# Optimization experiments

Hardware: AMD Instinct MI355X
Metric: run time of the kernel (lower is better)

## Reference

```python
import jax, jax.numpy as jnp
import numpy as np
import math

DIM = 1024
NUM_HEADS = 16
QUANTUM_HEADS = 2
HEAD_DIM = DIM // NUM_HEADS          # 64
TRAD_HEADS = NUM_HEADS - QUANTUM_HEADS  # 14
B, S = 1, 1024
STEPS = 2048
LN_EPS = 1e-5


def setup_inputs() -> dict:
    key = jax.random.key(0)
    ks = jax.random.split(key, 10)
    hd2 = 2 * HEAD_DIM
    return {
        "x": jax.random.normal(ks[0], (B, S, DIM), jnp.float32),
        # to_quantum_state: Linear(head_dim -> 2*head_dim) + LayerNorm + Tanh (shared across quantum heads)
        "qs_W": jax.random.normal(ks[1], (hd2, HEAD_DIM), jnp.float32) / math.sqrt(HEAD_DIM),
        "qs_b": jnp.zeros((hd2,), jnp.float32),
        "ln_g": jnp.ones((hd2,), jnp.float32),
        "ln_b": jnp.zeros((hd2,), jnp.float32),
        # per-quantum-head scalars
        "q_freq": jax.random.normal(ks[2], (QUANTUM_HEADS,), jnp.float32) * 0.02,
        "q_shift": jax.random.normal(ks[3], (QUANTUM_HEADS,), jnp.float32) * 0.02,
        # traditional head projections (no bias)
        "Wq": jax.random.normal(ks[4], (TRAD_HEADS * HEAD_DIM, DIM), jnp.float32) / math.sqrt(DIM),
        "Wk": jax.random.normal(ks[5], (TRAD_HEADS * HEAD_DIM, DIM), jnp.float32) / math.sqrt(DIM),
        "Wv": jax.random.normal(ks[6], (TRAD_HEADS * HEAD_DIM, DIM), jnp.float32) / math.sqrt(DIM),
        # output projection (with bias)
        "Wo": jax.random.normal(ks[7], (DIM, DIM), jnp.float32) / math.sqrt(DIM),
        "bo": jnp.zeros((DIM,), jnp.float32),
    }


def _layernorm(h, g, b):
    mu = jnp.mean(h, axis=-1, keepdims=True)
    var = jnp.mean(jnp.square(h - mu), axis=-1, keepdims=True)
    return (h - mu) * jax.lax.rsqrt(var + LN_EPS) * g + b


def _forward(x, qs_W, qs_b, ln_g, ln_b, q_freq, q_shift, Wq, Wk, Wv, Wo, bo):
    cos_table = jnp.cos(jnp.linspace(0.0, 2.0 * math.pi, STEPS).astype(jnp.float32))
    scale = 1.0 / math.sqrt(HEAD_DIM)
    two_pi = 2.0 * math.pi

    outs = []
    # ---- quantum heads (small fixed loop over structurally distinct heads) ----
    for h in range(QUANTUM_HEADS):
        xh = x[..., h * HEAD_DIM:(h + 1) * HEAD_DIM]          # (B,S,hd)
        qs = jnp.tanh(_layernorm(xh @ qs_W.T + qs_b, ln_g, ln_b))  # (B,S,2hd)
        amp, phase = jnp.split(qs, 2, axis=-1)                 # each (B,S,hd)
        # per (query pos i, key pos j, feature d) phase difference
        pd = (phase[:, :, None, :] - phase[:, None, :, :]) * q_freq[h] + q_shift[h]  # (B,S,S,hd)
        idx = jnp.floor(jnp.mod(pd / two_pi * STEPS, STEPS)).astype(jnp.int32)
        interf = cos_table[idx]                                # lookup-table gather, (B,S,S,hd)
        attn = jnp.einsum('bid,bjd,bijd->bij', amp, amp, interf) * scale
        attn = jax.nn.softmax(attn, axis=-1)
        outs.append(attn @ xh)                                 # (B,S,hd), values are the raw head slice

    # ---- traditional heads: standard multi-head attention ----
    q = (x @ Wq.T).reshape(B, S, TRAD_HEADS, HEAD_DIM)
    k = (x @ Wk.T).reshape(B, S, TRAD_HEADS, HEAD_DIM)
    v = (x @ Wv.T).reshape(B, S, TRAD_HEADS, HEAD_DIM)
    scores = jnp.einsum('bqhd,bkhd->bhqk', q, k) * scale       # (B,Ht,S,S)
    probs = jax.nn.softmax(scores, axis=-1)
    trad = jnp.einsum('bhqk,bkhd->bqhd', probs, v).reshape(B, S, TRAD_HEADS * HEAD_DIM)
    outs.append(trad)

    out = jnp.concatenate(outs, axis=-1)                       # (B,S,DIM)
    return out @ Wo.T + bo


def reference(x, qs_W, qs_b, ln_g, ln_b, q_freq, q_shift, Wq, Wk, Wv, Wo, bo):
    return _forward(x, qs_W, qs_b, ln_g, ln_b, q_freq, q_shift, Wq, Wk, Wv, Wo, bo)
```

## Files before the change

kernel.cpp:

```cpp
#include <hip/hip_runtime.h>
#include <hip/hip_bf16.h>
#include <math.h>

#define DIMX 1024
#define SEQ  1024
#define HD   64
#define QH   2
#define TH   14
#define QKVN 2688
#define LN_EPS 1e-5f
#define NB_F2B 4736
#define NB_QPREP 1024
#define NB_XT 32

typedef __bf16 bf16x8 __attribute__((ext_vector_type(8)));
typedef float  f32x4  __attribute__((ext_vector_type(4)));
typedef unsigned short u16x8 __attribute__((ext_vector_type(8)));

__device__ inline unsigned short f2b_rne(float f) {
  unsigned int u = __float_as_uint(f);
  unsigned int r = (u + 0x7FFF + ((u >> 16) & 1)) >> 16;
  return (unsigned short)r;
}

__device__ inline float waveRedSum(float v) {
  #pragma unroll
  for (int off = 32; off; off >>= 1) v += __shfl_xor(v, off, 64);
  return v;
}

__global__ __launch_bounds__(256) void k_prep(
    const float* __restrict__ x, const float* __restrict__ qsW,
    const float* __restrict__ qsb, const float* __restrict__ lng,
    const float* __restrict__ lnb, const float* __restrict__ qfreq,
    const float* __restrict__ qshift,
    const float* __restrict__ wq, const float* __restrict__ wk,
    const float* __restrict__ wv, const float* __restrict__ wo,
    unsigned short* __restrict__ x_bf, unsigned short* __restrict__ wqkv_bf,
    unsigned short* __restrict__ wo_bf,
    unsigned short* __restrict__ qcs, unsigned short* __restrict__ kcs,
    unsigned short* __restrict__ xt) {
  __shared__ float xrow2[2][HD];
  __shared__ float redm[2][2], redv[2][2];
  __shared__ float qsv2[2][128];
  __shared__ unsigned short ttile[64][72];
  int t = threadIdx.x;
  int bid = blockIdx.x;
  if (bid < NB_F2B) {
    long i = ((long)bid * 256 + t) * 4;
    float4 v;
    unsigned short* dst;
    if (i < 1048576) {
      v = *reinterpret_cast<const float4*>(x + i);
      dst = x_bf + i;
    } else if (i < 3801088) {
      long j = i - 1048576;
      const float* s = (j < 917504) ? wq + j
                     : (j < 1835008) ? wk + (j - 917504)
                                     : wv + (j - 1835008);
      v = *reinterpret_cast<const float4*>(s);
      dst = wqkv_bf + j;
    } else {
      long j = i - 3801088;
      v = *reinterpret_cast<const float4*>(wo + j);
      dst = wo_bf + j;
    }
    ushort4 o;
    o.x = f2b_rne(v.x); o.y = f2b_rne(v.y); o.z = f2b_rne(v.z); o.w = f2b_rne(v.w);
    *reinterpret_cast<ushort4*>(dst) = o;
  } else if (bid < NB_F2B + NB_QPREP) {
    int half = t >> 7, o = t & 127;
    int row = (bid - NB_F2B) * 2 + half;
    int h = row >> 10, i = row & 1023;
    if (o < HD) xrow2[half][o] = x[i * DIMX + h * HD + o];
    __syncthreads();
    float s = qsb[o];
    #pragma unroll
    for (int d = 0; d < HD; d += 4) {
      float4 w = *reinterpret_cast<const float4*>(qsW + o * HD + d);
      float4 xv = *reinterpret_cast<const float4*>(&xrow2[half][d]);
      s += xv.x * w.x + xv.y * w.y + xv.z * w.z + xv.w * w.w;
    }
    int wid = (o >> 6), lane = o & 63;
    float ws = waveRedSum(s);
    if (lane == 0) redm[half][wid] = ws;
    __syncthreads();
    float mu = (redm[half][0] + redm[half][1]) * (1.0f / 128.0f);
    float dv = s - mu;
    float ws2 = waveRedSum(dv * dv);
    if (lane == 0) redv[half][wid] = ws2;
    __syncthreads();
    float var = (redv[half][0] + redv[half][1]) * (1.0f / 128.0f);
    float y = dv * rsqrtf(var + LN_EPS) * lng[o] + lnb[o];
    qsv2[half][o] = tanhf(y);
    __syncthreads();
    float freq = qfreq[h], shift = qshift[h];
    size_t base = ((size_t)h * 1024 + i) * 128;
    if (o < HD) {
      float amp = qsv2[half][o];
      float a = qsv2[half][64 + o] * freq + shift;
      float sn, cs;
      __sincosf(a, &sn, &cs);
      qcs[base + o]      = f2b_rne(amp * cs);
      qcs[base + 64 + o] = f2b_rne(amp * sn);
    } else {
      int d = o - 64;
      float amp = qsv2[half][d];
      float bAng = qsv2[half][64 + d] * freq;
      float sn, cs;
      __sincosf(bAng, &sn, &cs);
      kcs[base + d]      = f2b_rne(amp * cs);
      kcs[base + 64 + d] = f2b_rne(amp * sn);
    }
  } else {
    int b = bid - (NB_F2B + NB_QPREP);
    int h = b >> 4, kv0 = (b & 15) * 64;
    #pragma unroll
    for (int pass = 0; pass < 2; ++pass) {
      int s = pass * 256 + t;
      int r = s >> 3, c8 = (s & 7) * 8;
      const float* src = x + (size_t)(kv0 + r) * DIMX + h * 64 + c8;
      float4 a = *reinterpret_cast<const float4*>(src);
      float4 b4 = *reinterpret_cast<const float4*>(src + 4);
      ushort4 o1, o2;
      o1.x = f2b_rne(a.x);  o1.y = f2b_rne(a.y);  o1.z = f2b_rne(a.z);  o1.w = f2b_rne(a.w);
      o2.x = f2b_rne(b4.x); o2.y = f2b_rne(b4.y); o2.z = f2b_rne(b4.z); o2.w = f2b_rne(b4.w);
      *reinterpret_cast<ushort4*>(&ttile[r][c8]) = o1;
      *reinterpret_cast<ushort4*>(&ttile[r][c8 + 4]) = o2;
    }
    __syncthreads();
    #pragma unroll
    for (int pass = 0; pass < 2; ++pass) {
      int s = pass * 256 + t;
      int d = s >> 3, k8 = (s & 7) * 8;
      u16x8 o;
      #pragma unroll
      for (int j = 0; j < 8; ++j) o[j] = ttile[k8 + j][d];
      *reinterpret_cast<u16x8*>(xt + (size_t)h * 65536 + (size_t)d * 1024 + kv0 + k8) = o;
    }
  }
}

template <int HAS_BIAS, int BF16_OUT>
__device__ __forceinline__ void dev_gemm64(
    char* smem,
    const unsigned short* __restrict__ A, const unsigned short* __restrict__ B,
    void* __restrict__ Cv, const float* __restrict__ bias,
    unsigned short* __restrict__ vtp,
    int bx, int by, int K, int lda, int ldb, int ldc) {
  unsigned short* As = (unsigned short*)smem;
  unsigned short* Bs = As + 64 * 128;
  int t = threadIdx.x, lane = t & 63, w = t >> 6;
  int wr = w >> 1, wc = w & 1;
  int g = lane >> 4, li = lane & 15;
  int mb = by * 64, nb = bx * 64;
  int rstg = t >> 4;
  int cs = t & 15;
  f32x4 acc[2][2] = {};
  for (int kb = 0; kb < K; kb += 128) {
    __syncthreads();
    #pragma unroll
    for (int i = 0; i < 4; ++i) {
      int row = i * 16 + rstg;
      int csw = ((cs ^ (row & 7)) * 8);
      __builtin_amdgcn_global_load_lds(
          (const __attribute__((address_space(1))) unsigned int*)(A + (size_t)(mb + row) * lda + kb + csw),
          (__attribute__((address_space(3))) unsigned int*)(As + row * 128 + cs * 8), 16, 0, 0);
      __builtin_amdgcn_global_load_lds(
          (const __attribute__((address_space(1))) unsigned int*)(B + (size_t)(nb + row) * ldb + kb + csw),
          (__attribute__((address_space(3))) unsigned int*)(Bs + row * 128 + cs * 8), 16, 0, 0);
    }
    __syncthreads();
    #pragma unroll
    for (int kk = 0; kk < 4; ++kk) {
      bf16x8 af[2], bfr[2];
      #pragma unroll
      for (int m = 0; m < 2; ++m) {
        int r = wr * 32 + m * 16 + li;
        int cb = kk * 4 + g;
        af[m] = *reinterpret_cast<const bf16x8*>(&As[r * 128 + ((cb ^ (r & 7)) * 8)]);
      }
      #pragma unroll
      for (int n = 0; n < 2; ++n) {
        int r = wc * 32 + n * 16 + li;
        int cb = kk * 4 + g;
        bfr[n] = *reinterpret_cast<const bf16x8*>(&Bs[r * 128 + ((cb ^ (r & 7)) * 8)]);
      }
      #pragma unroll
      for (int m = 0; m < 2; ++m)
        #pragma unroll
        for (int n = 0; n < 2; ++n)
          acc[m][n] = __builtin_amdgcn_mfma_f32_16x16x32_bf16(af[m], bfr[n], acc[m][n], 0, 0, 0);
    }
  }
  if (vtp != nullptr && nb >= 1792) {
    #pragma unroll
    for (int m = 0; m < 2; ++m) {
      int row0 = mb + wr * 32 + m * 16 + g * 4;
      #pragma unroll
      for (int n = 0; n < 2; ++n) {
        int colrel = nb - 1792 + wc * 32 + n * 16 + li;
        #pragma unroll
        for (int r = 0; r < 4; ++r)
          vtp[(size_t)colrel * 1024 + row0 + r] = f2b_rne(acc[m][n][r]);
      }
    }
    return;
  }
  #pragma unroll
  for (int m = 0; m < 2; ++m) {
    int row0 = mb + wr * 32 + m * 16 + g * 4;
    #pragma unroll
    for (int n = 0; n < 2; ++n) {
      int col = nb + wc * 32 + n * 16 + li;
      float bval = HAS_BIAS ? bias[col] : 0.0f;
      #pragma unroll
      for (int r = 0; r < 4; ++r) {
        size_t idx = (size_t)(row0 + r) * ldc + col;
        if (BF16_OUT) ((unsigned short*)Cv)[idx] = f2b_rne(acc[m][n][r] + bval);
        else          ((float*)Cv)[idx] = acc[m][n][r] + bval;
      }
    }
  }
}

__global__ __launch_bounds__(256) void k_qkv(
    const unsigned short* __restrict__ x_bf, const unsigned short* __restrict__ wqkv,
    unsigned short* __restrict__ qkv, unsigned short* __restrict__ vt) {
  __shared__ __align__(16) char smem[32768];
  int bid = blockIdx.x;
  int swz = (bid & 7) * 84 + (bid >> 3);
  int by = swz / 42, bx = swz % 42;
  dev_gemm64<0, 1>(smem, x_bf, wqkv, qkv, nullptr, vt, bx, by, DIMX, DIMX, DIMX, QKVN);
}

template <int DQK, int NT>
__device__ __forceinline__ void dev_fattn4(
    char* smem,
    const unsigned short* __restrict__ Qp, int ldq,
    const unsigned short* __restrict__ Kp, int ldk,
    const unsigned short* __restrict__ Vp,
    int q0, int kv0, int slot,
    float* __restrict__ pout, float* __restrict__ pml) {
  const int KREG = DQK / 32;
  const int NSLOT = DQK / 8;
  unsigned short* Ks = (unsigned short*)smem;
  unsigned short* Ps = Ks + 64 * DQK;
  int t = threadIdx.x, lane = t & 63, w = t >> 6;
  int g = lane >> 4, li = lane & 15;

  bf16x8 aq[KREG];
  #pragma unroll
  for (int kk = 0; kk < KREG; ++kk)
    aq[kk] = *reinterpret_cast<const bf16x8*>(
        Qp + (size_t)(q0 + w * 16 + li) * ldq + kk * 32 + g * 8);

  f32x4 s_all[NT][4] = {};

  {
    int rstg = t / NSLOT, cs = t % NSLOT;
    #pragma unroll
    for (int tile = 0; tile < NT; ++tile) {
      int j0 = kv0 + tile * 64;
      __syncthreads();
      #pragma unroll
      for (int i = 0; i < NSLOT / 4; ++i) {
        int row = i * (256 / NSLOT) + rstg;
        int csw = ((cs ^ (row & 7)) * 8);
        __builtin_amdgcn_global_load_lds(
            (const __attribute__((address_space(1))) unsigned int*)(Kp + (size_t)(j0 + row) * ldk + csw),
            (__attribute__((address_space(3))) unsigned int*)(Ks + row * DQK + cs * 8), 16, 0, 0);
      }
      __syncthreads();
      #pragma unroll
      for (int kk = 0; kk < KREG; ++kk) {
        #pragma unroll
        for (int n = 0; n < 4; ++n) {
          int r = n * 16 + li;
          int cb = kk * 4 + g;
          bf16x8 bk = *reinterpret_cast<const bf16x8*>(&Ks[r * DQK + ((cb ^ (r & 7)) * 8)]);
          s_all[tile][n] = __builtin_amdgcn_mfma_f32_16x16x32_bf16(aq[kk], bk, s_all[tile][n], 0, 0, 0);
        }
      }
    }
  }

  float mrow[4], lrow[4];
  #pragma unroll
  for (int r = 0; r < 4; ++r) {
    float tm = -1e30f;
    #pragma unroll
    for (int tile = 0; tile < NT; ++tile)
      #pragma unroll
      for (int n = 0; n < 4; ++n) tm = fmaxf(tm, s_all[tile][n][r]);
    #pragma unroll
    for (int m = 1; m < 16; m <<= 1) tm = fmaxf(tm, __shfl_xor(tm, m, 64));
    float rs = 0.f;
    #pragma unroll
    for (int tile = 0; tile < NT; ++tile)
      #pragma unroll
      for (int n = 0; n < 4; ++n) {
        float p = __expf((s_all[tile][n][r] - tm) * 0.125f);
        s_all[tile][n][r] = p;
        rs += p;
      }
    #pragma unroll
    for (int m = 1; m < 16; m <<= 1) rs += __shfl_xor(rs, m, 64);
    mrow[r] = tm; lrow[r] = rs;
  }

  f32x4 acc_o[4] = {};
  {
    int rstg = t >> 3, cs = t & 7;
    #pragma unroll
    for (int tile = 0; tile < NT; ++tile) {
      int j0 = kv0 + tile * 64;
      __syncthreads();
      #pragma unroll
      for (int i = 0; i < 2; ++i) {
        int row = i * 32 + rstg;
        int csw = ((cs ^ (row & 7)) * 8);
        __builtin_amdgcn_global_load_lds(
            (const __attribute__((address_space(1))) unsigned int*)(Vp + (size_t)row * 1024 + j0 + csw),
            (__attribute__((address_space(3))) unsigned int*)(Ks + row * 64 + cs * 8), 16, 0, 0);
      }
      __syncthreads();
      #pragma unroll
      for (int n = 0; n < 4; ++n)
        #pragma unroll
        for (int r = 0; r < 4; ++r)
          Ps[(w * 16 + g * 4 + r) * 72 + n * 16 + li] = f2b_rne(s_all[tile][n][r]);
      #pragma unroll
      for (int kk = 0; kk < 2; ++kk) {
        bf16x8 ap = *reinterpret_cast<const bf16x8*>(&Ps[(w * 16 + li) * 72 + kk * 32 + g * 8]);
        #pragma unroll
        for (int n = 0; n < 4; ++n) {
          int r = n * 16 + li;
          int cb = kk * 4 + g;
          bf16x8 bv = *reinterpret_cast<const bf16x8*>(&Ks[r * 64 + ((cb ^ (r & 7)) * 8)]);
          acc_o[n] = __builtin_amdgcn_mfma_f32_16x16x32_bf16(ap, bv, acc_o[n], 0, 0, 0);
        }
      }
    }
  }

  size_t rowbase = (size_t)slot * 1024;
  #pragma unroll
  for (int r = 0; r < 4; ++r) {
    int qr = q0 + w * 16 + g * 4 + r;
    #pragma unroll
    for (int n = 0; n < 4; ++n)
      pout[(rowbase + qr) * 64 + n * 16 + li] = acc_o[n][r];
    if (li == 0) {
      pml[(rowbase + qr) * 2 + 0] = mrow[r];
      pml[(rowbase + qr) * 2 + 1] = lrow[r];
    }
  }
}

__global__ __launch_bounds__(256) void k_attn_all(
    const unsigned short* __restrict__ qcs, const unsigned short* __restrict__ kcs,
    const unsigned short* __restrict__ xt, const unsigned short* __restrict__ qkv,
    const unsigned short* __restrict__ vt,
    float* __restrict__ pout, float* __restrict__ pml) {
  __shared__ __align__(16) char smem[25600];
  int bid = blockIdx.x;
  int l = (bid & 7) * 144 + (bid >> 3);
  if (l < 256) {
    int qt = l & 15, h = (l >> 4) & 1, split = l >> 5;
    dev_fattn4<128, 2>(smem, qcs + (size_t)h * SEQ * 128, 128,
                       kcs + (size_t)h * SEQ * 128, 128,
                       xt + (size_t)h * 65536,
                       qt * 64, split * 128, h * 8 + split, pout, pml);
  } else {
    int b2 = l - 256;
    int qt = b2 & 15, hs = b2 >> 4;
    int h = hs % 14, split = hs / 14;
    dev_fattn4<64, 4>(smem, qkv + h * 64, QKVN,
                      qkv + 896 + h * 64, QKVN,
                      vt + (size_t)h * 65536,
                      qt * 64, split * 256, 16 + h * 4 + split, pout, pml);
  }
}

__global__ __launch_bounds__(256) void k_fmerge(
    const float* __restrict__ pout, const float* __restrict__ pml,
    unsigned short* __restrict__ concat) {
  int rq = blockIdx.x * 4 + (threadIdx.x >> 6);
  int lh = rq >> 10, q = rq & 1023;
  int d = threadIdx.x & 63;
  int s0 = (lh < 2) ? lh * 8 : 16 + (lh - 2) * 4;
  int ns = (lh < 2) ? 8 : 4;
  float m_s[8], l_s[8];
  float M = -1e30f;
  #pragma unroll
  for (int s = 0; s < 8; ++s) {
    if (s < ns) {
      size_t rb = (size_t)(s0 + s) * 1024 + q;
      m_s[s] = pml[rb * 2 + 0];
      l_s[s] = pml[rb * 2 + 1];
      M = fmaxf(M, m_s[s]);
    }
  }
  float num = 0.f, den = 0.f;
  #pragma unroll
  for (int s = 0; s < 8; ++s) {
    if (s < ns) {
      float wgt = __expf((m_s[s] - M) * 0.125f);
      num += wgt * pout[((size_t)(s0 + s) * 1024 + q) * 64 + d];
      den += wgt * l_s[s];
    }
  }
  concat[(size_t)q * DIMX + lh * 64 + d] = f2b_rne(num / den);
}

__global__ __launch_bounds__(256) void k_oproj(
    const unsigned short* __restrict__ A, const unsigned short* __restrict__ B,
    float* __restrict__ C, const float* __restrict__ bias) {
  __shared__ unsigned short As[32 * 128];
  __shared__ unsigned short Bs[64 * 128];
  int bid = blockIdx.x;
  int swz = (bid & 7) * 64 + (bid >> 3);
  int by = swz >> 4, bx = swz & 15;
  int t = threadIdx.x, lane = t & 63, w = t >> 6;
  int wr = w & 1, wc = w >> 1;
  int g = lane >> 4, li = lane & 15;
  int mb = by * 32, nb = bx * 64;
  int rstg = t >> 4, cs = t & 15;
  f32x4 acc[2] = {};
  for (int kb = 0; kb < DIMX; kb += 128) {
    __syncthreads();
    #pragma unroll
    for (int i = 0; i < 2; ++i) {
      int row = i * 16 + rstg;
      int csw = ((cs ^ (row & 7)) * 8);
      __builtin_amdgcn_global_load_lds(
          (const __attribute__((address_space(1))) unsigned int*)(A + (size_t)(mb + row) * DIMX + kb + csw),
          (__attribute__((address_space(3))) unsigned int*)(As + row * 128 + cs * 8), 16, 0, 0);
    }
    #pragma unroll
    for (int i = 0; i < 4; ++i) {
      int row = i * 16 + rstg;
      int csw = ((cs ^ (row & 7)) * 8);
      __builtin_amdgcn_global_load_lds(
          (const __attribute__((address_space(1))) unsigned int*)(B + (size_t)(nb + row) * DIMX + kb + csw),
          (__attribute__((address_space(3))) unsigned int*)(Bs + row * 128 + cs * 8), 16, 0, 0);
    }
    __syncthreads();
    #pragma unroll
    for (int kk = 0; kk < 4; ++kk) {
      int cb = kk * 4 + g;
      int ra = wr * 16 + li;
      bf16x8 af = *reinterpret_cast<const bf16x8*>(&As[ra * 128 + ((cb ^ (ra & 7)) * 8)]);
      #pragma unroll
      for (int n = 0; n < 2; ++n) {
        int rb = wc * 32 + n * 16 + li;
        bf16x8 bfr = *reinterpret_cast<const bf16x8*>(&Bs[rb * 128 + ((cb ^ (rb & 7)) * 8)]);
        acc[n] = __builtin_amdgcn_mfma_f32_16x16x32_bf16(af, bfr, acc[n], 0, 0, 0);
      }
    }
  }
  int row0 = mb + wr * 16 + g * 4;
  #pragma unroll
  for (int n = 0; n < 2; ++n) {
    int col = nb + wc * 32 + n * 16 + li;
    float bval = bias[col];
    #pragma unroll
    for (int r = 0; r < 4; ++r)
      C[(size_t)(row0 + r) * DIMX + col] = acc[n][r] + bval;
  }
}

extern "C" void kernel_launch(void* const* d_in, const int* in_sizes, int n_in,
                              void* d_out, int out_size, void* d_ws, size_t ws_size,
                              hipStream_t stream) {
  const float* x      = (const float*)d_in[0];
  const float* qsW    = (const float*)d_in[1];
  const float* qsb    = (const float*)d_in[2];
  const float* lng    = (const float*)d_in[3];
  const float* lnb    = (const float*)d_in[4];
  const float* qfreq  = (const float*)d_in[5];
  const float* qshift = (const float*)d_in[6];
  const float* Wq     = (const float*)d_in[7];
  const float* Wk     = (const float*)d_in[8];
  const float* Wv     = (const float*)d_in[9];
  const float* Wo     = (const float*)d_in[10];
  const float* bo     = (const float*)d_in[11];
  float* out = (float*)d_out;

  char* ws = (char*)d_ws;
  size_t off = 0;
  auto alloc = [&](size_t bytes) { char* p = ws + off; off += (bytes + 255) & ~(size_t)255; return p; };
  unsigned short* x_bf      = (unsigned short*)alloc((size_t)SEQ * DIMX * 2);
  unsigned short* wqkv_bf   = (unsigned short*)alloc((size_t)QKVN * DIMX * 2);
  unsigned short* wo_bf     = (unsigned short*)alloc((size_t)DIMX * DIMX * 2);
  unsigned short* concat_bf = (unsigned short*)alloc((size_t)SEQ * DIMX * 2);
  unsigned short* qkv_bf    = (unsigned short*)alloc((size_t)SEQ * QKVN * 2);
  unsigned short* qcs       = (unsigned short*)alloc((size_t)QH * SEQ * 128 * 2);
  unsigned short* kcs       = (unsigned short*)alloc((size_t)QH * SEQ * 128 * 2);
  unsigned short* vt        = (unsigned short*)alloc((size_t)TH * HD * SEQ * 2);
  unsigned short* xt        = (unsigned short*)alloc((size_t)QH * HD * SEQ * 2);
  float*          pout      = (float*)alloc((size_t)72 * SEQ * 64 * 4);
  float*          pml       = (float*)alloc((size_t)72 * SEQ * 2 * 4);

  k_prep<<<NB_F2B + NB_QPREP + NB_XT, 256, 0, stream>>>(
      x, qsW, qsb, lng, lnb, qfreq, qshift, Wq, Wk, Wv, Wo,
      x_bf, wqkv_bf, wo_bf, qcs, kcs, xt);

  k_qkv<<<672, 256, 0, stream>>>(x_bf, wqkv_bf, qkv_bf, vt);

  k_attn_all<<<1152, 256, 0, stream>>>(qcs, kcs, xt, qkv_bf, vt, pout, pml);

  k_fmerge<<<16 * SEQ / 4, 256, 0, stream>>>(pout, pml, concat_bf);

  k_oproj<<<512, 256, 0, stream>>>(concat_bf, wo_bf, out, bo);
}
```

Before: 73.66 us.

## Enlarge attention blocks to 128 queries so 8 waves share K/V tiles

The fused attention kernel now runs 512-thread blocks covering 128 query rows instead of 256-thread blocks covering 64. Each K and V tile staged in LDS is reused by 8 waves rather than 4, and K and V are staged in larger 16KB chunks. This roughly halves the global-to-LDS traffic per query and the number of barrier rounds. The trade-off is half as many blocks (576), a larger LDS footprint per block, and possibly lower occupancy or worse load balance.

After: 75.72 us. +2.8%, slower.

```diff
diff --git a/kernel.cpp b/kernel.cpp
--- a/kernel.cpp
+++ b/kernel.cpp
@@ -234,8 +234,8 @@
   dev_gemm64<0, 1>(smem, x_bf, wqkv, qkv, nullptr, vt, bx, by, DIMX, DIMX, DIMX, QKVN);
 }
 
-template <int DQK, int NT>
-__device__ __forceinline__ void dev_fattn4(
+template <int DQK, int KVR>
+__device__ __forceinline__ void dev_fattn5(
     char* smem,
     const unsigned short* __restrict__ Qp, int ldq,
     const unsigned short* __restrict__ Kp, int ldk,
@@ -243,9 +243,12 @@
     int q0, int kv0, int slot,
     float* __restrict__ pout, float* __restrict__ pml) {
   const int KREG = DQK / 32;
+  const int NC = KVR / 16;
+  const int KSR = 16384 / (DQK * 2);
   const int NSLOT = DQK / 8;
+  const int RPI = 512 / NSLOT;
   unsigned short* Ks = (unsigned short*)smem;
-  unsigned short* Ps = Ks + 64 * DQK;
+  unsigned short* Ps = Ks + 8192;
   int t = threadIdx.x, lane = t & 63, w = t >> 6;
   int g = lane >> 4, li = lane & 15;
 
@@ -255,31 +258,31 @@
     aq[kk] = *reinterpret_cast<const bf16x8*>(
         Qp + (size_t)(q0 + w * 16 + li) * ldq + kk * 32 + g * 8);
 
-  f32x4 s_all[NT][4] = {};
+  f32x4 s_all[NC] = {};
 
   {
     int rstg = t / NSLOT, cs = t % NSLOT;
     #pragma unroll
-    for (int tile = 0; tile < NT; ++tile) {
-      int j0 = kv0 + tile * 64;
+    for (int s = 0; s < KVR / KSR; ++s) {
       __syncthreads();
       #pragma unroll
-      for (int i = 0; i < NSLOT / 4; ++i) {
-        int row = i * (256 / NSLOT) + rstg;
+      for (int i = 0; i < KSR / RPI; ++i) {
+        int row = i * RPI + rstg;
         int csw = ((cs ^ (row & 7)) * 8);
         __builtin_amdgcn_global_load_lds(
-            (const __attribute__((address_space(1))) unsigned int*)(Kp + (size_t)(j0 + row) * ldk + csw),
+            (const __attribute__((address_space(1))) unsigned int*)(Kp + (size_t)(kv0 + s * KSR + row) * ldk + csw),
             (__attribute__((address_space(3))) unsigned int*)(Ks + row * DQK + cs * 8), 16, 0, 0);
       }
       __syncthreads();
       #pragma unroll
-      for (int kk = 0; kk < KREG; ++kk) {
+      for (int cl = 0; cl < KSR / 16; ++cl) {
+        int c = s * (KSR / 16) + cl;
+        int r = cl * 16 + li;
         #pragma unroll
-        for (int n = 0; n < 4; ++n) {
-          int r = n * 16 + li;
+        for (int kk = 0; kk < KREG; ++kk) {
           int cb = kk * 4 + g;
           bf16x8 bk = *reinterpret_cast<const bf16x8*>(&Ks[r * DQK + ((cb ^ (r & 7)) * 8)]);
-          s_all[tile][n] = __builtin_amdgcn_mfma_f32_16x16x32_bf16(aq[kk], bk, s_all[tile][n], 0, 0, 0);
+          s_all[c] = __builtin_amdgcn_mfma_f32_16x16x32_bf16(aq[kk], bk, s_all[c], 0, 0, 0);
         }
       }
     }
@@ -290,20 +293,16 @@
   for (int r = 0; r < 4; ++r) {
     float tm = -1e30f;
     #pragma unroll
-    for (int tile = 0; tile < NT; ++tile)
-      #pragma unroll
-      for (int n = 0; n < 4; ++n) tm = fmaxf(tm, s_all[tile][n][r]);
+    for (int c = 0; c < NC; ++c) tm = fmaxf(tm, s_all[c][r]);
     #pragma unroll
     for (int m = 1; m < 16; m <<= 1) tm = fmaxf(tm, __shfl_xor(tm, m, 64));
     float rs = 0.f;
     #pragma unroll
-    for (int tile = 0; tile < NT; ++tile)
-      #pragma unroll
-      for (int n = 0; n < 4; ++n) {
-        float p = __expf((s_all[tile][n][r] - tm) * 0.125f);
-        s_all[tile][n][r] = p;
-        rs += p;
-      }
+    for (int c = 0; c < NC; ++c) {
+      float p = __expf((s_all[c][r] - tm) * 0.125f);
+      s_all[c][r] = p;
+      rs += p;
+    }
     #pragma unroll
     for (int m = 1; m < 16; m <<= 1) rs += __shfl_xor(rs, m, 64);
     mrow[r] = tm; lrow[r] = rs;
@@ -311,34 +310,37 @@
 
   f32x4 acc_o[4] = {};
   {
-    int rstg = t >> 3, cs = t & 7;
-    #pragma unroll
-    for (int tile = 0; tile < NT; ++tile) {
-      int j0 = kv0 + tile * 64;
+    int rstg = t >> 4, cs = t & 15;
+    #pragma unroll
+    for (int sv = 0; sv < KVR / 128; ++sv) {
       __syncthreads();
       #pragma unroll
       for (int i = 0; i < 2; ++i) {
         int row = i * 32 + rstg;
         int csw = ((cs ^ (row & 7)) * 8);
         __builtin_amdgcn_global_load_lds(
-            (const __attribute__((address_space(1))) unsigned int*)(Vp + (size_t)row * 1024 + j0 + csw),
-            (__attribute__((address_space(3))) unsigned int*)(Ks + row * 64 + cs * 8), 16, 0, 0);
+            (const __attribute__((address_space(1))) unsigned int*)(Vp + (size_t)row * 1024 + kv0 + sv * 128 + csw),
+            (__attribute__((address_space(3))) unsigned int*)(Ks + row * 128 + cs * 8), 16, 0, 0);
       }
       __syncthreads();
       #pragma unroll
-      for (int n = 0; n < 4; ++n)
+      for (int half = 0; half < 2; ++half) {
+        int cbase = sv * 8 + half * 4;
         #pragma unroll
-        for (int r = 0; r < 4; ++r)
-          Ps[(w * 16 + g * 4 + r) * 72 + n * 16 + li] = f2b_rne(s_all[tile][n][r]);
-      #pragma unroll
-      for (int kk = 0; kk < 2; ++kk) {
-        bf16x8 ap = *reinterpret_cast<const bf16x8*>(&Ps[(w * 16 + li) * 72 + kk * 32 + g * 8]);
+        for (int n4 = 0; n4 < 4; ++n4)
+          #pragma unroll
+          for (int r = 0; r < 4; ++r)
+            Ps[(w * 16 + g * 4 + r) * 72 + n4 * 16 + li] = f2b_rne(s_all[cbase + n4][r]);
         #pragma unroll
-        for (int n = 0; n < 4; ++n) {
-          int r = n * 16 + li;
-          int cb = kk * 4 + g;
-          bf16x8 bv = *reinterpret_cast<const bf16x8*>(&Ks[r * 64 + ((cb ^ (r & 7)) * 8)]);
-          acc_o[n] = __builtin_amdgcn_mfma_f32_16x16x32_bf16(ap, bv, acc_o[n], 0, 0, 0);
+        for (int kk = 0; kk < 2; ++kk) {
+          bf16x8 ap = *reinterpret_cast<const bf16x8*>(&Ps[(w * 16 + li) * 72 + kk * 32 + g * 8]);
+          #pragma unroll
+          for (int n = 0; n < 4; ++n) {
+            int r = n * 16 + li;
+            int cb = half * 8 + kk * 4 + g;
+            bf16x8 bv = *reinterpret_cast<const bf16x8*>(&Ks[r * 128 + ((cb ^ (r & 7)) * 8)]);
+            acc_o[n] = __builtin_amdgcn_mfma_f32_16x16x32_bf16(ap, bv, acc_o[n], 0, 0, 0);
+          }
         }
       }
     }
@@ -358,28 +360,28 @@
   }
 }
 
-__global__ __launch_bounds__(256) void k_attn_all(
+__global__ __launch_bounds__(512) void k_attn_all(
     const unsigned short* __restrict__ qcs, const unsigned short* __restrict__ kcs,
     const unsigned short* __restrict__ xt, const unsigned short* __restrict__ qkv,
     const unsigned short* __restrict__ vt,
     float* __restrict__ pout, float* __restrict__ pml) {
-  __shared__ __align__(16) char smem[25600];
+  __shared__ __align__(16) char smem[34816];
   int bid = blockIdx.x;
-  int l = (bid & 7) * 144 + (bid >> 3);
-  if (l < 256) {
-    int qt = l & 15, h = (l >> 4) & 1, split = l >> 5;
-    dev_fattn4<128, 2>(smem, qcs + (size_t)h * SEQ * 128, 128,
-                       kcs + (size_t)h * SEQ * 128, 128,
-                       xt + (size_t)h * 65536,
-                       qt * 64, split * 128, h * 8 + split, pout, pml);
+  int l = (bid & 7) * 72 + (bid >> 3);
+  if (l < 128) {
+    int qt = l & 7, h = (l >> 3) & 1, split = l >> 4;
+    dev_fattn5<128, 128>(smem, qcs + (size_t)h * SEQ * 128, 128,
+                         kcs + (size_t)h * SEQ * 128, 128,
+                         xt + (size_t)h * 65536,
+                         qt * 128, split * 128, h * 8 + split, pout, pml);
   } else {
-    int b2 = l - 256;
-    int qt = b2 & 15, hs = b2 >> 4;
+    int l2 = l - 128;
+    int qt = l2 & 7, hs = l2 >> 3;
     int h = hs % 14, split = hs / 14;
-    dev_fattn4<64, 4>(smem, qkv + h * 64, QKVN,
-                      qkv + 896 + h * 64, QKVN,
-                      vt + (size_t)h * 65536,
-                      qt * 64, split * 256, 16 + h * 4 + split, pout, pml);
+    dev_fattn5<64, 256>(smem, qkv + h * 64, QKVN,
+                        qkv + 896 + h * 64, QKVN,
+                        vt + (size_t)h * 65536,
+                        qt * 128, split * 256, 16 + h * 4 + split, pout, pml);
   }
 }
 
@@ -509,7 +511,7 @@
 
   k_qkv<<<672, 256, 0, stream>>>(x_bf, wqkv_bf, qkv_bf, vt);
 
-  k_attn_all<<<1152, 256, 0, stream>>>(qcs, kcs, xt, qkv_bf, vt, pout, pml);
+  k_attn_all<<<576, 512, 0, stream>>>(qcs, kcs, xt, qkv_bf, vt, pout, pml);
 
   k_fmerge<<<16 * SEQ / 4, 256, 0, stream>>>(pout, pml, concat_bf);
 
```

## Store attention partials in bf16 and shrink K staging LDS footprint

Applied to the files above, without the earlier changes.

Partial attention outputs written by the attention kernel and read by the merge kernel are now stored as bf16 instead of fp32, halving that intermediate traffic. The K-tile staging for the 128-wide quantum heads now uses 32-row stages instead of 64-row ones, so LDS shrinks from 25.6KB to 17KB per block, which may allow more resident blocks per CU. The cost is extra barriers for the quantum-head path and reduced precision of the unnormalized partial outputs before merging.

After: 78.07 us. 1.06x slower.

```diff
diff --git a/kernel.cpp b/kernel.cpp
--- a/kernel.cpp
+++ b/kernel.cpp
@@ -21,6 +21,9 @@
   unsigned int u = __float_as_uint(f);
   unsigned int r = (u + 0x7FFF + ((u >> 16) & 1)) >> 16;
   return (unsigned short)r;
+}
+__device__ inline float b2f(unsigned short u) {
+  return __uint_as_float((unsigned int)u << 16);
 }
 
 __device__ inline float waveRedSum(float v) {
@@ -241,11 +244,16 @@
     const unsigned short* __restrict__ Kp, int ldk,
     const unsigned short* __restrict__ Vp,
     int q0, int kv0, int slot,
-    float* __restrict__ pout, float* __restrict__ pml) {
+    unsigned short* __restrict__ pout, float* __restrict__ pml) {
   const int KREG = DQK / 32;
   const int NSLOT = DQK / 8;
+  const int SR = (DQK == 128) ? 32 : 64;
+  const int NSTG = (NT * 64) / SR;
+  const int CLS = SR / 16;
+  const int RPI = 256 / NSLOT;
+  const int NC = NT * 4;
   unsigned short* Ks = (unsigned short*)smem;
-  unsigned short* Ps = Ks + 64 * DQK;
+  unsigned short* Ps = Ks + 4096;
   int t = threadIdx.x, lane = t & 63, w = t >> 6;
   int g = lane >> 4, li = lane & 15;
 
@@ -255,31 +263,31 @@
     aq[kk] = *reinterpret_cast<const bf16x8*>(
         Qp + (size_t)(q0 + w * 16 + li) * ldq + kk * 32 + g * 8);
 
-  f32x4 s_all[NT][4] = {};
+  f32x4 s_all[NC] = {};
 
   {
     int rstg = t / NSLOT, cs = t % NSLOT;
     #pragma unroll
-    for (int tile = 0; tile < NT; ++tile) {
-      int j0 = kv0 + tile * 64;
+    for (int s = 0; s < NSTG; ++s) {
       __syncthreads();
       #pragma unroll
-      for (int i = 0; i < NSLOT / 4; ++i) {
-        int row = i * (256 / NSLOT) + rstg;
+      for (int i = 0; i < SR / RPI; ++i) {
+        int row = i * RPI + rstg;
         int csw = ((cs ^ (row & 7)) * 8);
         __builtin_amdgcn_global_load_lds(
-            (const __attribute__((address_space(1))) unsigned int*)(Kp + (size_t)(j0 + row) * ldk + csw),
+            (const __attribute__((address_space(1))) unsigned int*)(Kp + (size_t)(kv0 + s * SR + row) * ldk + csw),
             (__attribute__((address_space(3))) unsigned int*)(Ks + row * DQK + cs * 8), 16, 0, 0);
       }
       __syncthreads();
       #pragma unroll
-      for (int kk = 0; kk < KREG; ++kk) {
+      for (int cl = 0; cl < CLS; ++cl) {
+        int c = s * CLS + cl;
+        int r = cl * 16 + li;
         #pragma unroll
-        for (int n = 0; n < 4; ++n) {
-          int r = n * 16 + li;
+        for (int kk = 0; kk < KREG; ++kk) {
           int cb = kk * 4 + g;
           bf16x8 bk = *reinterpret_cast<const bf16x8*>(&Ks[r * DQK + ((cb ^ (r & 7)) * 8)]);
-          s_all[tile][n] = __builtin_amdgcn_mfma_f32_16x16x32_bf16(aq[kk], bk, s_all[tile][n], 0, 0, 0);
+          s_all[c] = __builtin_amdgcn_mfma_f32_16x16x32_bf16(aq[kk], bk, s_all[c], 0, 0, 0);
         }
       }
     }
@@ -290,20 +298,16 @@
   for (int r = 0; r < 4; ++r) {
     float tm = -1e30f;
     #pragma unroll
-    for (int tile = 0; tile < NT; ++tile)
-      #pragma unroll
-      for (int n = 0; n < 4; ++n) tm = fmaxf(tm, s_all[tile][n][r]);
+    for (int c = 0; c < NC; ++c) tm = fmaxf(tm, s_all[c][r]);
     #pragma unroll
     for (int m = 1; m < 16; m <<= 1) tm = fmaxf(tm, __shfl_xor(tm, m, 64));
     float rs = 0.f;
     #pragma unroll
-    for (int tile = 0; tile < NT; ++tile)
-      #pragma unroll
-      for (int n = 0; n < 4; ++n) {
-        float p = __expf((s_all[tile][n][r] - tm) * 0.125f);
-        s_all[tile][n][r] = p;
-        rs += p;
-      }
+    for (int c = 0; c < NC; ++c) {
+      float p = __expf((s_all[c][r] - tm) * 0.125f);
+      s_all[c][r] = p;
+      rs += p;
+    }
     #pragma unroll
     for (int m = 1; m < 16; m <<= 1) rs += __shfl_xor(rs, m, 64);
     mrow[r] = tm; lrow[r] = rs;
@@ -313,8 +317,8 @@
   {
     int rstg = t >> 3, cs = t & 7;
     #pragma unroll
-    for (int tile = 0; tile < NT; ++tile) {
-      int j0 = kv0 + tile * 64;
+    for (int sv = 0; sv < NT; ++sv) {
+      int j0 = kv0 + sv * 64;
       __syncthreads();
       #pragma unroll
       for (int i = 0; i < 2; ++i) {
@@ -326,10 +330,10 @@
       }
       __syncthreads();
       #pragma unroll
-      for (int n = 0; n < 4; ++n)
+      for (int n4 = 0; n4 < 4; ++n4)
         #pragma unroll
         for (int r = 0; r < 4; ++r)
-          Ps[(w * 16 + g * 4 + r) * 72 + n * 16 + li] = f2b_rne(s_all[tile][n][r]);
+          Ps[(w * 16 + g * 4 + r) * 72 + n4 * 16 + li] = f2b_rne(s_all[sv * 4 + n4][r]);
       #pragma unroll
       for (int kk = 0; kk < 2; ++kk) {
         bf16x8 ap = *reinterpret_cast<const bf16x8*>(&Ps[(w * 16 + li) * 72 + kk * 32 + g * 8]);
@@ -350,7 +354,7 @@
     int qr = q0 + w * 16 + g * 4 + r;
     #pragma unroll
     for (int n = 0; n < 4; ++n)
-      pout[(rowbase + qr) * 64 + n * 16 + li] = acc_o[n][r];
+      pout[(rowbase + qr) * 64 + n * 16 + li] = f2b_rne(acc_o[n][r]);
     if (li == 0) {
       pml[(rowbase + qr) * 2 + 0] = mrow[r];
       pml[(rowbase + qr) * 2 + 1] = lrow[r];
@@ -362,8 +366,8 @@
     const unsigned short* __restrict__ qcs, const unsigned short* __restrict__ kcs,
     const unsigned short* __restrict__ xt, const unsigned short* __restrict__ qkv,
     const unsigned short* __restrict__ vt,
-    float* __restrict__ pout, float* __restrict__ pml) {
-  __shared__ __align__(16) char smem[25600];
+    unsigned short* __restrict__ pout, float* __restrict__ pml) {
+  __shared__ __align__(16) char smem[17408];
   int bid = blockIdx.x;
   int l = (bid & 7) * 144 + (bid >> 3);
   if (l < 256) {
@@ -384,7 +388,7 @@
 }
 
 __global__ __launch_bounds__(256) void k_fmerge(
-    const float* __restrict__ pout, const float* __restrict__ pml,
+    const unsigned short* __restrict__ pout, const float* __restrict__ pml,
     unsigned short* __restrict__ concat) {
   int rq = blockIdx.x * 4 + (threadIdx.x >> 6);
   int lh = rq >> 10, q = rq & 1023;
@@ -407,7 +411,7 @@
   for (int s = 0; s < 8; ++s) {
     if (s < ns) {
       float wgt = __expf((m_s[s] - M) * 0.125f);
-      num += wgt * pout[((size_t)(s0 + s) * 1024 + q) * 64 + d];
+      num += wgt * b2f(pout[((size_t)(s0 + s) * 1024 + q) * 64 + d]);
       den += wgt * l_s[s];
     }
   }
@@ -500,7 +504,7 @@
   unsigned short* kcs       = (unsigned short*)alloc((size_t)QH * SEQ * 128 * 2);
   unsigned short* vt        = (unsigned short*)alloc((size_t)TH * HD * SEQ * 2);
   unsigned short* xt        = (unsigned short*)alloc((size_t)QH * HD * SEQ * 2);
-  float*          pout      = (float*)alloc((size_t)72 * SEQ * 64 * 4);
+  unsigned short* pout      = (unsigned short*)alloc((size_t)72 * SEQ * 64 * 2);
   float*          pml       = (float*)alloc((size_t)72 * SEQ * 2 * 4);
 
   k_prep<<<NB_F2B + NB_QPREP + NB_XT, 256, 0, stream>>>(
```

## Double-buffer K/V tiles with async global-to-LDS loads in traditional-head attention

Applied to the files above, without the earlier changes.

Adds a new attention device routine for the traditional heads. It streams 64-row K and V tiles into two LDS buffers with direct global-to-LDS loads, so the next tile's load overlaps the current tile's MFMA work. All four score tiles stay in registers, and the softmax is computed once before the PV pass. This is meant to hide global load latency. In exchange it holds more registers (16 accumulator vectors for scores) and relies on hand-placed waitcnt and barriers.

After: 73.40 us. No clear change (-0.4%).

```diff
diff --git a/kernel.cpp b/kernel.cpp
--- a/kernel.cpp
+++ b/kernel.cpp
@@ -358,6 +358,139 @@
   }
 }
 
+#define ISSUE_K(TILE, BUF) { \
+  int j0_ = kv0 + (TILE) * 64; \
+  _Pragma("unroll") \
+  for (int i_ = 0; i_ < 2; ++i_) { \
+    int row_ = i_ * 32 + rk; \
+    int csw_ = ((ck ^ (row_ & 7)) * 8); \
+    __builtin_amdgcn_global_load_lds( \
+        (const __attribute__((address_space(1))) unsigned int*)(Kp + (size_t)(j0_ + row_) * ldk + csw_), \
+        (__attribute__((address_space(3))) unsigned int*)((BUF) + row_ * 64 + ck * 8), 16, 0, 0); \
+  } }
+
+#define ISSUE_V(TILE, BUF) { \
+  int j0_ = kv0 + (TILE) * 64; \
+  _Pragma("unroll") \
+  for (int i_ = 0; i_ < 2; ++i_) { \
+    int row_ = i_ * 32 + rk; \
+    int csw_ = ((ck ^ (row_ & 7)) * 8); \
+    __builtin_amdgcn_global_load_lds( \
+        (const __attribute__((address_space(1))) unsigned int*)(Vp + (size_t)row_ * 1024 + j0_ + csw_), \
+        (__attribute__((address_space(3))) unsigned int*)((BUF) + row_ * 64 + ck * 8), 16, 0, 0); \
+  } }
+
+#define MFMA_K(TILE, BUF) { \
+  _Pragma("unroll") \
+  for (int kk_ = 0; kk_ < 2; ++kk_) { \
+    _Pragma("unroll") \
+    for (int n_ = 0; n_ < 4; ++n_) { \
+      int r_ = n_ * 16 + li; \
+      int cb_ = kk_ * 4 + g; \
+      bf16x8 bk_ = *reinterpret_cast<const bf16x8*>(&(BUF)[r_ * 64 + ((cb_ ^ (r_ & 7)) * 8)]); \
+      s_all[TILE][n_] = __builtin_amdgcn_mfma_f32_16x16x32_bf16(aq[kk_], bk_, s_all[TILE][n_], 0, 0, 0); \
+    } } }
+
+#define PV_T(TILE, BUF) { \
+  _Pragma("unroll") \
+  for (int n4_ = 0; n4_ < 4; ++n4_) \
+    _Pragma("unroll") \
+    for (int r_ = 0; r_ < 4; ++r_) \
+      Ps[(w * 16 + g * 4 + r_) * 72 + n4_ * 16 + li] = f2b_rne(s_all[TILE][n4_][r_]); \
+  _Pragma("unroll") \
+  for (int kk_ = 0; kk_ < 2; ++kk_) { \
+    bf16x8 ap_ = *reinterpret_cast<const bf16x8*>(&Ps[(w * 16 + li) * 72 + kk_ * 32 + g * 8]); \
+    _Pragma("unroll") \
+    for (int n_ = 0; n_ < 4; ++n_) { \
+      int r_ = n_ * 16 + li; \
+      int cb_ = kk_ * 4 + g; \
+      bf16x8 bv_ = *reinterpret_cast<const bf16x8*>(&(BUF)[r_ * 64 + ((cb_ ^ (r_ & 7)) * 8)]); \
+      acc_o[n_] = __builtin_amdgcn_mfma_f32_16x16x32_bf16(ap_, bv_, acc_o[n_], 0, 0, 0); \
+    } } }
+
+#define WAITBAR2() { asm volatile("s_waitcnt vmcnt(2)" ::: "memory"); \
+  __builtin_amdgcn_sched_barrier(0); __builtin_amdgcn_s_barrier(); \
+  __builtin_amdgcn_sched_barrier(0); }
+#define WAITBAR0() { asm volatile("s_waitcnt vmcnt(0)" ::: "memory"); \
+  __builtin_amdgcn_sched_barrier(0); __builtin_amdgcn_s_barrier(); \
+  __builtin_amdgcn_sched_barrier(0); }
+#define REBAR() { __builtin_amdgcn_sched_barrier(0); __builtin_amdgcn_s_barrier(); \
+  __builtin_amdgcn_sched_barrier(0); }
+
+__device__ __forceinline__ void dev_fattn_db(
+    char* smem,
+    const unsigned short* __restrict__ Qp, int ldq,
+    const unsigned short* __restrict__ Kp, int ldk,
+    const unsigned short* __restrict__ Vp,
+    int q0, int kv0, int slot,
+    float* __restrict__ pout, float* __restrict__ pml) {
+  unsigned short* B0 = (unsigned short*)smem;
+  unsigned short* B1 = B0 + 4096;
+  unsigned short* Ps = B0 + 8192;
+  int t = threadIdx.x, lane = t & 63, w = t >> 6;
+  int g = lane >> 4, li = lane & 15;
+  int rk = t >> 3, ck = t & 7;
+
+  bf16x8 aq[2];
+  #pragma unroll
+  for (int kk = 0; kk < 2; ++kk)
+    aq[kk] = *reinterpret_cast<const bf16x8*>(
+        Qp + (size_t)(q0 + w * 16 + li) * ldq + kk * 32 + g * 8);
+
+  f32x4 s_all[4][4] = {};
+  f32x4 acc_o[4] = {};
+
+  ISSUE_K(0, B0);
+  ISSUE_K(1, B1);
+
+  WAITBAR2(); MFMA_K(0, B0); REBAR(); ISSUE_K(2, B0);
+  WAITBAR2(); MFMA_K(1, B1); REBAR(); ISSUE_K(3, B1);
+  WAITBAR2(); MFMA_K(2, B0); REBAR(); ISSUE_V(0, B0);
+  WAITBAR2(); MFMA_K(3, B1); REBAR(); ISSUE_V(1, B1);
+
+  float mrow[4], lrow[4];
+  #pragma unroll
+  for (int r = 0; r < 4; ++r) {
+    float tm = -1e30f;
+    #pragma unroll
+    for (int tile = 0; tile < 4; ++tile)
+      #pragma unroll
+      for (int n = 0; n < 4; ++n) tm = fmaxf(tm, s_all[tile][n][r]);
+    #pragma unroll
+    for (int m = 1; m < 16; m <<= 1) tm = fmaxf(tm, __shfl_xor(tm, m, 64));
+    float rs = 0.f;
+    #pragma unroll
+    for (int tile = 0; tile < 4; ++tile)
+      #pragma unroll
+      for (int n = 0; n < 4; ++n) {
+        float p = __expf((s_all[tile][n][r] - tm) * 0.125f);
+        s_all[tile][n][r] = p;
+        rs += p;
+      }
+    #pragma unroll
+    for (int m = 1; m < 16; m <<= 1) rs += __shfl_xor(rs, m, 64);
+    mrow[r] = tm; lrow[r] = rs;
+  }
+
+  WAITBAR2(); PV_T(0, B0); REBAR(); ISSUE_V(2, B0);
+  WAITBAR2(); PV_T(1, B1); REBAR(); ISSUE_V(3, B1);
+  WAITBAR2(); PV_T(2, B0);
+  WAITBAR0(); PV_T(3, B1);
+
+  size_t rowbase = (size_t)slot * 1024;
+  #pragma unroll
+  for (int r = 0; r < 4; ++r) {
+    int qr = q0 + w * 16 + g * 4 + r;
+    #pragma unroll
+    for (int n = 0; n < 4; ++n)
+      pout[(rowbase + qr) * 64 + n * 16 + li] = acc_o[n][r];
+    if (li == 0) {
+      pml[(rowbase + qr) * 2 + 0] = mrow[r];
+      pml[(rowbase + qr) * 2 + 1] = lrow[r];
+    }
+  }
+}
+
 __global__ __launch_bounds__(256) void k_attn_all(
     const unsigned short* __restrict__ qcs, const unsigned short* __restrict__ kcs,
     const unsigned short* __restrict__ xt, const unsigned short* __restrict__ qkv,
@@ -376,10 +509,10 @@
     int b2 = l - 256;
     int qt = b2 & 15, hs = b2 >> 4;
     int h = hs % 14, split = hs / 14;
-    dev_fattn4<64, 4>(smem, qkv + h * 64, QKVN,
-                      qkv + 896 + h * 64, QKVN,
-                      vt + (size_t)h * 65536,
-                      qt * 64, split * 256, 16 + h * 4 + split, pout, pml);
+    dev_fattn_db(smem, qkv + h * 64, QKVN,
+                 qkv + 896 + h * 64, QKVN,
+                 vt + (size_t)h * 65536,
+                 qt * 64, split * 256, 16 + h * 4 + split, pout, pml);
   }
 }
 
```
